# Performance work log

Measured on AMD Instinct MI355X. Metric: run time of the kernel, lower is better.

The kernel has to match this reference:

```python
import jax, jax.numpy as jnp
import numpy as np

N = 100000   # nodes
E = 1600000  # edges


def setup_inputs() -> dict:
    key = jax.random.key(0)
    ks = jax.random.split(key, 9)
    return {
        "in_feat": jax.random.normal(ks[0], (N, 256), jnp.float32),
        "W": jax.random.normal(ks[1], (256, 128), jnp.float32) * 0.05,
        "attn_l": jax.random.normal(ks[2], (1, 128), jnp.float32) * 0.1,
        "attn_r": jax.random.normal(ks[3], (1, 128), jnp.float32) * 0.1,
        "bias": jax.random.normal(ks[4], (1, 128), jnp.float32) * 0.01,
        "fc_w": jax.random.normal(ks[5], (128, 2), jnp.float32) * 0.1,
        "fc_b": jax.random.normal(ks[6], (2,), jnp.float32) * 0.01,
        "src": jax.random.randint(ks[7], (E,), 0, N, jnp.int32),
        "dst": jax.random.randint(ks[8], (E,), 0, N, jnp.int32),
    }


def reference(in_feat, W, attn_l, attn_r, bias, fc_w, fc_b, src, dst):
    # GATConv, num_heads=1 (head dim kept implicit since it is squeezed anyway)
    h = in_feat @ W                              # [N, F] projected features
    el = jnp.sum(h * attn_l, axis=-1)            # [N] left attention logits
    er = jnp.sum(h * attn_r, axis=-1)            # [N] right attention logits
    e = jax.nn.leaky_relu(el[src] + er[dst], negative_slope=0.2)  # [E]
    # edge softmax segmented by destination node (numerically stable)
    m = jax.ops.segment_max(e, dst, num_segments=N)               # [N]
    ex = jnp.exp(e - m[dst])                                      # [E]
    s = jax.ops.segment_sum(ex, dst, num_segments=N)              # [N]
    alpha = ex / jnp.where(s == 0, 1.0, s)[dst]                   # [E]
    # attention-weighted aggregation of source features to destinations
    agg = jax.ops.segment_sum(alpha[:, None] * h[src], dst, num_segments=N)  # [N, F]
    agg = agg + bias                                              # GATConv bias
    # head: ReLU -> Linear -> sigmoid
    out = jax.nn.sigmoid(jax.nn.relu(agg) @ fc_w + fc_b)          # [N, C]
    return out
```

## Files before the change

kernel.cpp:

```cpp
#include <hip/hip_runtime.h>
#include <cstdint>
#include <cstddef>

#define N_NODES 100000
#define E_EDGES 1600000
#define F_IN 256
#define F_OUT 128
#define NBKT 391
#define OBCAP 5120
#define GEMM_NB 1563
#define WCVT_NB 128
#define HSTR 400

#define GLOBAL_AS __attribute__((address_space(1)))
#define LDS_AS    __attribute__((address_space(3)))

typedef __attribute__((ext_vector_type(8))) short  short8v;
typedef __attribute__((ext_vector_type(4))) float  float4v;

__device__ __forceinline__ unsigned short f2bf(float x) {
    union { float f; unsigned u; } v; v.f = x;
    unsigned r = v.u + 0x7fffu + ((v.u >> 16) & 1u);
    return (unsigned short)(r >> 16);
}

__device__ __forceinline__ unsigned cvt_pk_bf16(float lo, float hi) {
    unsigned r;
    asm("v_cvt_pk_bf16_f32 %0, %1, %2" : "=v"(r) : "v"(lo), "v"(hi));
    return r;
}

__global__ __launch_bounds__(256) void wcvt_hist(const float* __restrict__ W,
                                                 unsigned short* __restrict__ Wt,
                                                 const int* __restrict__ dst,
                                                 int* __restrict__ bcnt,
                                                 int* __restrict__ hist) {
    __shared__ int h[NBKT];
    int t = threadIdx.x;
    if (blockIdx.x < WCVT_NB) {
        int i = blockIdx.x * 256 + t;
        int k = i >> 7, j = i & 127;
        Wt[j * F_IN + k] = f2bf(W[i]);
        return;
    }
    int b = blockIdx.x - WCVT_NB;
    for (int i = t; i < NBKT; i += 256) h[i] = 0;
    __syncthreads();
    int e0  = b * 4096;
    int end = min(e0 + 4096, E_EDGES);
    for (int i = e0 + t; i < end; i += 256) atomicAdd(&h[dst[i] >> 8], 1);
    __syncthreads();
    for (int i = t; i < NBKT; i += 256) {
        int c = h[i];
        hist[b * HSTR + i] = c;
        if (c) atomicAdd(&bcnt[i], c);
    }
}

__global__ __launch_bounds__(512) void k_scan2(const int* __restrict__ bcnt,
                                               int* __restrict__ bbase,
                                               int* __restrict__ hist) {
    __shared__ int s[512];
    __shared__ int base_sh;
    int t = threadIdx.x;
    int i = blockIdx.x;
    int d = (t < NBKT) ? bcnt[t] : 0;
    s[t] = d;
    __syncthreads();
    for (int off = 1; off < 512; off <<= 1) {
        int v = (t >= off) ? s[t - off] : 0;
        __syncthreads();
        s[t] += v;
        __syncthreads();
    }
    if (t == 0) {
        int bi = (i > 0) ? s[i - 1] : 0;
        base_sh = bi;
        bbase[i] = bi;
        if (i == NBKT - 1) bbase[NBKT] = s[NBKT - 1];
    }
    __syncthreads();
    int base_i = base_sh;
    int hv = (t < NBKT) ? hist[t * HSTR + i] : 0;
    __syncthreads();
    s[t] = hv;
    __syncthreads();
    for (int off = 1; off < 512; off <<= 1) {
        int v = (t >= off) ? s[t - off] : 0;
        __syncthreads();
        s[t] += v;
        __syncthreads();
    }
    if (t < NBKT) hist[t * HSTR + i] = s[t] - hv + base_i;
}

__global__ __launch_bounds__(256) void gemm_scatter(const float* __restrict__ A,
                                                    const unsigned short* __restrict__ Wt,
                                                    const float* __restrict__ attn_l,
                                                    const float* __restrict__ attn_r,
                                                    unsigned short* __restrict__ Hb,
                                                    float* __restrict__ el,
                                                    float* __restrict__ er,
                                                    const int* __restrict__ src,
                                                    const int* __restrict__ dst,
                                                    const int* __restrict__ hist,
                                                    unsigned int* __restrict__ epack) {
    __shared__ char smem[32 * 1024];
    int tid = threadIdx.x;

    if (blockIdx.x >= GEMM_NB) {
        int* h = (int*)smem;
        int b = blockIdx.x - GEMM_NB;
        for (int i = tid; i < NBKT; i += 256) h[i] = hist[b * HSTR + i];
        __syncthreads();
        int e0  = b * 4096;
        int end = min(e0 + 4096, E_EDGES);
        #pragma unroll
        for (int j = 0; j < 16; ++j) {
            int i = e0 + j * 256 + tid;
            if (i < end) {
                int dv = dst[i];
                int p = atomicAdd(&h[dv >> 8], 1);
                epack[p] = (unsigned)src[i] | ((unsigned)(dv & 255) << 17);
            }
        }
        return;
    }

    float*          Afs = (float*)smem;
    unsigned short* Bs  = (unsigned short*)(smem + 16 * 1024);
    int wave = tid >> 6, lane = tid & 63;
    int g = lane >> 4, c = lane & 15;
    int row0 = blockIdx.x * 64;
    float4v acc[8] = {};

    int a_r[4], a_k[4], a_w[4];
    #pragma unroll
    for (int i = 0; i < 4; ++i) {
        int W_ = i * 1024 + tid * 4;
        int r  = W_ >> 6;
        a_w[i] = W_;
        a_r[i] = min(row0 + r, N_NODES - 1);
        a_k[i] = (W_ & 63) ^ ((r & 15) << 2);
    }
    int b_j[4], b_k[4], b_u[4];
    #pragma unroll
    for (int i = 0; i < 4; ++i) {
        int U_ = i * 2048 + tid * 8;
        int j  = U_ >> 6;
        b_u[i] = U_;
        b_j[i] = j;
        b_k[i] = (U_ & 63) ^ ((j & 7) << 3);
    }

    for (int k0 = 0; k0 < F_IN; k0 += 64) {
        #pragma unroll
        for (int i = 0; i < 4; ++i) {
            __builtin_amdgcn_global_load_lds(
                (const GLOBAL_AS unsigned int*)(A + (size_t)a_r[i] * F_IN + k0 + a_k[i]),
                (LDS_AS unsigned int*)&Afs[a_w[i]], 16, 0, 0);
        }
        #pragma unroll
        for (int i = 0; i < 4; ++i) {
            __builtin_amdgcn_global_load_lds(
                (const GLOBAL_AS unsigned int*)(Wt + (size_t)b_j[i] * F_IN + k0 + b_k[i]),
                (LDS_AS unsigned int*)&Bs[b_u[i]], 16, 0, 0);
        }
        __syncthreads();
        int arow = wave * 16 + c;
        int aswz = (arow & 15) << 2;
        #pragma unroll
        for (int ks = 0; ks < 2; ++ks) {
            int woff = arow * 64 + ks * 32 + g * 8;
            float4 a0 = *reinterpret_cast<float4*>(&Afs[(woff)     ^ aswz]);
            float4 a1 = *reinterpret_cast<float4*>(&Afs[(woff + 4) ^ aswz]);
            unsigned u[4];
            u[0] = cvt_pk_bf16(a0.x, a0.y);
            u[1] = cvt_pk_bf16(a0.z, a0.w);
            u[2] = cvt_pk_bf16(a1.x, a1.y);
            u[3] = cvt_pk_bf16(a1.z, a1.w);
            short8v af = *reinterpret_cast<short8v*>(u);
            #pragma unroll
            for (int nt = 0; nt < 8; ++nt) {
                int j = nt * 16 + c;
                int boff = (j * 64 + ks * 32 + g * 8) ^ ((j & 7) << 3);
                short8v bf = *reinterpret_cast<short8v*>(&Bs[boff]);
                acc[nt] = __builtin_amdgcn_mfma_f32_16x16x32_bf16(af, bf, acc[nt], 0, 0, 0);
            }
        }
        __syncthreads();
    }

    float al[8], ar[8];
    #pragma unroll
    for (int nt = 0; nt < 8; ++nt) {
        al[nt] = attn_l[nt * 16 + c];
        ar[nt] = attn_r[nt * 16 + c];
    }
    #pragma unroll
    for (int r = 0; r < 4; ++r) {
        int grow = row0 + wave * 16 + g * 4 + r;
        float sl = 0.f, sr = 0.f;
        #pragma unroll
        for (int nt = 0; nt < 8; ++nt) {
            float h = acc[nt][r];
            sl += h * al[nt];
            sr += h * ar[nt];
        }
        if (grow < N_NODES) {
            #pragma unroll
            for (int nt = 0; nt < 8; ++nt)
                Hb[(size_t)grow * F_OUT + nt * 16 + c] = f2bf(acc[nt][r]);
        }
        #pragma unroll
        for (int off = 1; off < 16; off <<= 1) {
            sl += __shfl_xor(sl, off);
            sr += __shfl_xor(sr, off);
        }
        if (c == 0 && grow < N_NODES) { el[grow] = sl; er[grow] = sr; }
    }
}

__global__ __launch_bounds__(256) void k_sort2(const unsigned int* __restrict__ epack,
                                               const int* __restrict__ bbase,
                                               const float* __restrict__ el,
                                               const float* __restrict__ er,
                                               float2* __restrict__ exs,
                                               int* __restrict__ rowptr,
                                               int* __restrict__ deg) {
    __shared__ int hist[256], cur[256], s[256];
    __shared__ float ssl[256];
    __shared__ unsigned obuf[OBCAP];
    __shared__ float exb[OBCAP];
    int b = blockIdx.x, t = threadIdx.x;
    int base = bbase[b], end = bbase[b + 1];
    int cnt  = end - base;
    hist[t] = 0;
    ssl[t] = 0.f;
    __syncthreads();
    for (int i = t; i < cnt; i += 256) atomicAdd(&hist[epack[base + i] >> 17], 1);
    __syncthreads();
    int d = hist[t];
    s[t] = d;
    __syncthreads();
    for (int off = 1; off < 256; off <<= 1) {
        int v = (t >= off) ? s[t - off] : 0;
        __syncthreads();
        s[t] += v;
        __syncthreads();
    }
    int excl = s[t] - d;
    int n = b * 256 + t;
    if (n < N_NODES) { deg[n] = d; rowptr[n] = base + excl; }
    cur[t] = excl;
    __syncthreads();
    for (int i = t; i < cnt; i += 256) {
        unsigned e = epack[base + i];
        int d2  = e >> 17;
        int sid = (int)(e & 0x1FFFFu);
        float tv = el[sid] + er[b * 256 + d2];
        tv = tv > 0.f ? tv : 0.2f * tv;
        float ex = __expf(tv);
        int p = atomicAdd(&cur[d2], 1);
        if (p < OBCAP) { obuf[p] = e; exb[p] = ex; }
        atomicAdd(&ssl[d2], ex);
    }
    __syncthreads();
    for (int i = t; i < cnt; i += 256) {
        unsigned e = obuf[i];
        float alpha = exb[i] / ssl[e >> 17];
        exs[base + i] = make_float2(alpha, __uint_as_float((e & 0x1FFFFu) << 8));
    }
}

__global__ __launch_bounds__(256) void agg_fused(const int* __restrict__ rowptr,
                                                 const int* __restrict__ deg,
                                                 const float2* __restrict__ exs,
                                                 const char* __restrict__ Hc,
                                                 const float* __restrict__ bias,
                                                 const float* __restrict__ fcw,
                                                 const float* __restrict__ fcb,
                                                 float* __restrict__ out) {
    __shared__ float2 exbuf[4][64];
    int tid   = threadIdx.x;
    int wslot = tid >> 6;
    int wid   = (blockIdx.x * 256 + tid) >> 6;
    int lane  = tid & 63;
    if (wid >= N_NODES) return;
    int grp = lane >> 4, fl = lane & 15;
    int start = rowptr[wid];
    int dg    = deg[wid];
    float acc[8] = {};
    float2* eb = exbuf[wslot];
    unsigned flb = (unsigned)fl << 4;

    for (int base = 0; base < dg; base += 64) {
        int cnt = min(64, dg - base);
        float2 p2 = make_float2(0.f, 0.f);
        if (lane < cnt) p2 = exs[start + base + lane];
        eb[lane] = p2;
        __builtin_amdgcn_wave_barrier();
        int nq = (cnt + 3) >> 2;
        #pragma unroll 2
        for (int q = 0; q < nq; ++q) {
            float2 p = eb[q * 4 + grp];
            float aq = p.x;
            uint4 v = *(const uint4*)(Hc + (__float_as_uint(p.y) + flb));
            acc[0] += aq * __uint_as_float(v.x << 16);
            acc[1] += aq * __uint_as_float(v.x & 0xffff0000u);
            acc[2] += aq * __uint_as_float(v.y << 16);
            acc[3] += aq * __uint_as_float(v.y & 0xffff0000u);
            acc[4] += aq * __uint_as_float(v.z << 16);
            acc[5] += aq * __uint_as_float(v.z & 0xffff0000u);
            acc[6] += aq * __uint_as_float(v.w << 16);
            acc[7] += aq * __uint_as_float(v.w & 0xffff0000u);
        }
        __builtin_amdgcn_wave_barrier();
    }

    #pragma unroll
    for (int j = 0; j < 8; ++j) {
        acc[j] += __shfl_xor(acc[j], 16);
        acc[j] += __shfl_xor(acc[j], 32);
    }

    float4 b0 = ((const float4*)bias)[fl * 2];
    float4 b1 = ((const float4*)bias)[fl * 2 + 1];
    float d0 = 0.f, d1 = 0.f;
    #pragma unroll
    for (int j = 0; j < 8; ++j) {
        float bj = j < 4 ? (&b0.x)[j] : (&b1.x)[j - 4];
        float vv = fmaxf(acc[j] + bj, 0.f);
        float2 wj = ((const float2*)fcw)[fl * 8 + j];
        d0 += vv * wj.x;
        d1 += vv * wj.y;
    }
    #pragma unroll
    for (int off = 1; off < 16; off <<= 1) {
        d0 += __shfl_xor(d0, off);
        d1 += __shfl_xor(d1, off);
    }
    if (lane == 0) {
        out[(size_t)wid * 2 + 0] = 1.f / (1.f + __expf(-(d0 + fcb[0])));
        out[(size_t)wid * 2 + 1] = 1.f / (1.f + __expf(-(d1 + fcb[1])));
    }
}

extern "C" void kernel_launch(void* const* d_in, const int* in_sizes, int n_in,
                              void* d_out, int out_size, void* d_ws, size_t ws_size,
                              hipStream_t stream) {
    const float* in_feat = (const float*)d_in[0];
    const float* W       = (const float*)d_in[1];
    const float* attn_l  = (const float*)d_in[2];
    const float* attn_r  = (const float*)d_in[3];
    const float* bias    = (const float*)d_in[4];
    const float* fc_w    = (const float*)d_in[5];
    const float* fc_b    = (const float*)d_in[6];
    const int*   src     = (const int*)d_in[7];
    const int*   dst     = (const int*)d_in[8];
    float* out = (float*)d_out;

    char* p = (char*)d_ws;
    unsigned short* HB = (unsigned short*)p; p += (size_t)N_NODES * F_OUT * sizeof(unsigned short);
    unsigned short* WT = (unsigned short*)p; p += (size_t)F_IN * F_OUT * sizeof(unsigned short);
    float* EL     = (float*)p; p += (size_t)N_NODES * sizeof(float);
    float* ER     = (float*)p; p += (size_t)N_NODES * sizeof(float);
    int*   DEG    = (int*)p;   p += (size_t)N_NODES * sizeof(int);
    int*   ROWPTR = (int*)p;   p += (size_t)N_NODES * sizeof(int);
    int*   BCNT   = (int*)p;   p += 512 * sizeof(int);
    int*   BBASE  = (int*)p;   p += 512 * sizeof(int);
    int*   HIST   = (int*)p;   p += (size_t)NBKT * HSTR * sizeof(int);
    unsigned int* EPACK = (unsigned int*)p; p += (size_t)E_EDGES * sizeof(unsigned int);
    float2* EXS   = (float2*)p; p += (size_t)E_EDGES * sizeof(float2);

    hipMemsetAsync(BCNT, 0, 512 * sizeof(int), stream);

    wcvt_hist<<<WCVT_NB + NBKT, 256, 0, stream>>>(W, WT, dst, BCNT, HIST);
    k_scan2  <<<NBKT, 512, 0, stream>>>(BCNT, BBASE, HIST);
    gemm_scatter<<<GEMM_NB + NBKT, 256, 0, stream>>>(
        in_feat, WT, attn_l, attn_r, HB, EL, ER, src, dst, HIST, EPACK);
    k_sort2  <<<NBKT, 256, 0, stream>>>(EPACK, BBASE, EL, ER, EXS, ROWPTR, DEG);

    agg_fused<<<(N_NODES * 64 + 255) / 256, 256, 0, stream>>>(
        ROWPTR, DEG, EXS, (const char*)HB, bias, fc_w, fc_b, out);
}
```

Baseline: 145.9 us.

## Load full A tile into LDS once and read W fragments from global

The GEMM part now stages the whole 64x256 fp32 A tile into 64 KB of LDS in a single pass with one barrier, replacing the four-step K loop that had two barriers per step. The bf16 weight fragments are no longer staged in LDS; each lane reads them straight from global memory, relying on the small W staying in cache. This removes barrier stalls and LDS traffic for B. In exchange it uses more LDS per block, which can lower occupancy, and each MFMA now waits on a global load latency.

```diff
diff --git a/kernel.cpp b/kernel.cpp
--- a/kernel.cpp
+++ b/kernel.cpp
@@ -105,11 +105,11 @@
                                                     const int* __restrict__ dst,
                                                     const int* __restrict__ hist,
                                                     unsigned int* __restrict__ epack) {
-    __shared__ char smem[32 * 1024];
+    __shared__ __align__(16) float Afs[64 * 256];
     int tid = threadIdx.x;
 
     if (blockIdx.x >= GEMM_NB) {
-        int* h = (int*)smem;
+        int* h = (int*)Afs;
         int b = blockIdx.x - GEMM_NB;
         for (int i = tid; i < NBKT; i += 256) h[i] = hist[b * HSTR + i];
         __syncthreads();
@@ -127,68 +127,44 @@
         return;
     }
 
-    float*          Afs = (float*)smem;
-    unsigned short* Bs  = (unsigned short*)(smem + 16 * 1024);
     int wave = tid >> 6, lane = tid & 63;
     int g = lane >> 4, c = lane & 15;
     int row0 = blockIdx.x * 64;
     float4v acc[8] = {};
 
-    int a_r[4], a_k[4], a_w[4];
-    #pragma unroll
-    for (int i = 0; i < 4; ++i) {
+    #pragma unroll
+    for (int i = 0; i < 16; ++i) {
         int W_ = i * 1024 + tid * 4;
-        int r  = W_ >> 6;
-        a_w[i] = W_;
-        a_r[i] = min(row0 + r, N_NODES - 1);
-        a_k[i] = (W_ & 63) ^ ((r & 15) << 2);
-    }
-    int b_j[4], b_k[4], b_u[4];
-    #pragma unroll
-    for (int i = 0; i < 4; ++i) {
-        int U_ = i * 2048 + tid * 8;
-        int j  = U_ >> 6;
-        b_u[i] = U_;
-        b_j[i] = j;
-        b_k[i] = (U_ & 63) ^ ((j & 7) << 3);
-    }
-
-    for (int k0 = 0; k0 < F_IN; k0 += 64) {
+        int r  = W_ >> 8;
+        int kl = W_ & 255;
+        int ks = kl ^ ((r & 15) << 2);
+        int gr = min(row0 + r, N_NODES - 1);
+        __builtin_amdgcn_global_load_lds(
+            (const GLOBAL_AS unsigned int*)(A + (size_t)gr * F_IN + ks),
+            (LDS_AS unsigned int*)&Afs[W_], 16, 0, 0);
+    }
+    __syncthreads();
+
+    int arow = wave * 16 + c;
+    int aswz = (arow & 15) << 2;
+    const unsigned short* __restrict__ bcol = Wt + (size_t)c * F_IN;
+    #pragma unroll 2
+    for (int q = 0; q < 8; ++q) {
+        int woff = arow * 256 + q * 32 + g * 8;
+        float4 a0 = *reinterpret_cast<float4*>(&Afs[(woff)     ^ aswz]);
+        float4 a1 = *reinterpret_cast<float4*>(&Afs[(woff + 4) ^ aswz]);
+        unsigned u[4];
+        u[0] = cvt_pk_bf16(a0.x, a0.y);
+        u[1] = cvt_pk_bf16(a0.z, a0.w);
+        u[2] = cvt_pk_bf16(a1.x, a1.y);
+        u[3] = cvt_pk_bf16(a1.z, a1.w);
+        short8v af = *reinterpret_cast<short8v*>(u);
+        int koff = q * 32 + g * 8;
         #pragma unroll
-        for (int i = 0; i < 4; ++i) {
-            __builtin_amdgcn_global_load_lds(
-                (const GLOBAL_AS unsigned int*)(A + (size_t)a_r[i] * F_IN + k0 + a_k[i]),
-                (LDS_AS unsigned int*)&Afs[a_w[i]], 16, 0, 0);
-        }
-        #pragma unroll
-        for (int i = 0; i < 4; ++i) {
-            __builtin_amdgcn_global_load_lds(
-                (const GLOBAL_AS unsigned int*)(Wt + (size_t)b_j[i] * F_IN + k0 + b_k[i]),
-                (LDS_AS unsigned int*)&Bs[b_u[i]], 16, 0, 0);
-        }
-        __syncthreads();
-        int arow = wave * 16 + c;
-        int aswz = (arow & 15) << 2;
-        #pragma unroll
-        for (int ks = 0; ks < 2; ++ks) {
-            int woff = arow * 64 + ks * 32 + g * 8;
-            float4 a0 = *reinterpret_cast<float4*>(&Afs[(woff)     ^ aswz]);
-            float4 a1 = *reinterpret_cast<float4*>(&Afs[(woff + 4) ^ aswz]);
-            unsigned u[4];
-            u[0] = cvt_pk_bf16(a0.x, a0.y);
-            u[1] = cvt_pk_bf16(a0.z, a0.w);
-            u[2] = cvt_pk_bf16(a1.x, a1.y);
-            u[3] = cvt_pk_bf16(a1.z, a1.w);
-            short8v af = *reinterpret_cast<short8v*>(u);
-            #pragma unroll
-            for (int nt = 0; nt < 8; ++nt) {
-                int j = nt * 16 + c;
-                int boff = (j * 64 + ks * 32 + g * 8) ^ ((j & 7) << 3);
-                short8v bf = *reinterpret_cast<short8v*>(&Bs[boff]);
-                acc[nt] = __builtin_amdgcn_mfma_f32_16x16x32_bf16(af, bf, acc[nt], 0, 0, 0);
-            }
-        }
-        __syncthreads();
+        for (int nt = 0; nt < 8; ++nt) {
+            short8v bf = *reinterpret_cast<const short8v*>(bcol + (size_t)nt * 16 * F_IN + koff);
+            acc[nt] = __builtin_amdgcn_mfma_f32_16x16x32_bf16(af, bf, acc[nt], 0, 0, 0);
+        }
     }
 
     float al[8], ar[8];
```

Measured after the change: 182.7 us. 1.25x slower.
